# Kernel optimization log

Hardware: AMD Instinct MI355X
Metric: run time of the kernel (lower is better)

The kernel has to match this reference:

```python
import jax, jax.numpy as jnp
import numpy as np

N = 50000        # nodes
E = 800000       # edges (avg degree 16)
NFEAT = 16       # 14 feat + 2 pos
NHID = 64
NCLASS = 1
NGRAPHS = 500
NLAYERS = 5
DT, ALPHA, GAMMA = 1.0, 1.0, 1.0


def _lin_init(k, fan_in, fan_out):
    # torch nn.Linear default: U(-1/sqrt(fan_in), 1/sqrt(fan_in))
    lim = 1.0 / np.sqrt(fan_in)
    kw, kb = jax.random.split(k)
    W = jax.random.uniform(kw, (fan_in, fan_out), minval=-lim, maxval=lim, dtype=jnp.float32)
    b = jax.random.uniform(kb, (fan_out,), minval=-lim, maxval=lim, dtype=jnp.float32)
    return W, b


def setup_inputs() -> dict:
    key = jax.random.key(0)
    ks = jax.random.split(key, 8)
    x = jax.random.normal(ks[0], (N, 14), dtype=jnp.float32)
    pos = jax.random.normal(ks[1], (N, 2), dtype=jnp.float32)
    edge_index = jax.random.randint(ks[2], (2, E), 0, N, dtype=jnp.int64)
    batch = jnp.sort(jax.random.randint(ks[3], (N,), 0, NGRAPHS, dtype=jnp.int64))
    enc_W, enc_b = _lin_init(ks[4], NFEAT, NHID)
    conv_W, conv_b = _lin_init(ks[5], NHID, NHID)
    res_W, res_b = _lin_init(ks[6], NHID, NHID)
    dec_W, dec_b = _lin_init(ks[7], NHID, NCLASS)
    return dict(x=x, pos=pos, edge_index=edge_index, batch=batch,
                enc_W=enc_W, enc_b=enc_b, conv_W=conv_W, conv_b=conv_b,
                res_W=res_W, res_b=res_b, dec_W=dec_W, dec_b=dec_b)


def _gcn_conv(h, src, dst, W, b):
    # PyG GCNConv: add self-loops, symmetric normalization, scatter-add to dst.
    loop = jnp.arange(N, dtype=src.dtype)
    src2 = jnp.concatenate([src, loop])
    dst2 = jnp.concatenate([dst, loop])
    deg = jax.ops.segment_sum(jnp.ones_like(dst2, dtype=h.dtype), dst2, num_segments=N)
    dinv = jnp.where(deg > 0, jax.lax.rsqrt(deg), 0.0)
    hW = h @ W                                   # [N, nhid]
    norm = dinv[src2] * dinv[dst2]               # [E+N]
    msg = hW[src2] * norm[:, None]               # [E+N, nhid]
    return jax.ops.segment_sum(msg, dst2, num_segments=N) + b


def reference(x, pos, edge_index, batch, enc_W, enc_b, conv_W, conv_b, res_W, res_b, dec_W, dec_b):
    src, dst = edge_index[0], edge_index[1]
    inp = jnp.concatenate([x, pos], axis=-1)     # [N, nfeat]
    Y = inp @ enc_W + enc_b
    X = Y
    # dropout p=0 -> identity (eval mode)
    for _ in range(NLAYERS):
        agg = _gcn_conv(X, src, dst, conv_W, conv_b) + (X @ res_W + res_b)
        Y = Y + DT * (jax.nn.relu(agg) - ALPHA * Y - GAMMA * X)
        X = X + DT * Y
    Xo = X @ dec_W + dec_b                       # [N, 1]
    pooled = jax.ops.segment_sum(Xo, batch, num_segments=NGRAPHS)  # [G, 1]
    return pooled.squeeze(-1)                    # [G]
```

## Files before the change

kernel.cpp:

```cpp
#include <hip/hip_runtime.h>

#define NN 50000
#define NE 800000
#define NH 64
#define NG 500
#define NPAD 50176
#define NBKT 782
#define CAP 1536

__device__ __forceinline__ unsigned short f2bf(float f) {
  unsigned x = __float_as_uint(f);
  unsigned r = ((x >> 16) & 1u) + 0x7fffu;
  return (unsigned short)((x + r) >> 16);
}
__device__ __forceinline__ float bf2f(unsigned short u) {
  return __uint_as_float(((unsigned)u) << 16);
}


__global__ __launch_bounds__(256) void k_bin(const int* __restrict__ src, const int* __restrict__ dst,
                                             int* __restrict__ bcur, int* __restrict__ colp) {
  __shared__ int hist[NBKT];
  __shared__ int gbase[NBKT];
  int t = threadIdx.x;
  for (int b = t; b < NBKT; b += 256) hist[b] = 0;
  __syncthreads();
  int e0 = blockIdx.x * 8192;
#pragma unroll
  for (int i = 0; i < 32; i++) {
    int e = e0 + i * 256 + t;
    if (e < NE) atomicAdd(&hist[dst[e] >> 6], 1);
  }
  __syncthreads();
  for (int b = t; b < NBKT; b += 256) {
    int c = hist[b];
    gbase[b] = c ? atomicAdd(&bcur[b], c) : 0;
    hist[b] = 0;
  }
  __syncthreads();
#pragma unroll
  for (int i = 0; i < 32; i++) {
    int e = e0 + i * 256 + t;
    if (e < NE) {
      int s = src[e], d = dst[e];
      int b = d >> 6;
      int r = atomicAdd(&hist[b], 1);
      colp[b * CAP + gbase[b] + r] = (s << 6) | (d & 63);
    }
  }
}


__global__ __launch_bounds__(256) void k_csr(const int* __restrict__ bcur, const int* __restrict__ colp,
                                             int* __restrict__ cols, float* __restrict__ dinv,
                                             int* __restrict__ rowst, int* __restrict__ rowen,
                                             const int* __restrict__ batch, int* __restrict__ gptr) {
  __shared__ int hist[64];
  __shared__ int excl[65];
  int t = threadIdx.x;
  int b = blockIdx.x;

  int tid = b * 256 + t;
  if (tid < NN) {
    int bi = batch[tid];
    int bp = (tid > 0) ? batch[tid - 1] : -1;
    for (int g = bp + 1; g <= bi; g++) gptr[g] = tid;
    if (tid == NN - 1) {
      for (int g = bi + 1; g <= NG; g++) gptr[g] = NN;
    }
  }

  int base = b * CAP;
  int cnt = bcur[b];
  if (t < 64) hist[t] = 0;
  __syncthreads();
  for (int e = t; e < cnt; e += 256) atomicAdd(&hist[colp[base + e] & 63], 1);
  __syncthreads();
  if (t == 0) {
    int run = 0;
#pragma unroll
    for (int i = 0; i < 64; i++) { excl[i] = run; run += hist[i]; }
    excl[64] = run;
  }
  __syncthreads();
  if (t < 64) {
    int n = b * 64 + t;
    rowst[n] = base + excl[t];
    rowen[n] = base + excl[t + 1];
    if (n < NN) dinv[n] = rsqrtf((float)(hist[t] + 1));
    hist[t] = 0;
  }
  __syncthreads();
  for (int e = t; e < cnt; e += 256) {
    int w = colp[base + e];
    int d = w & 63;
    int r = atomicAdd(&hist[d], 1);
    cols[base + excl[d] + r] = w >> 6;
  }
}


__global__ __launch_bounds__(256) void k_encoder(const float* __restrict__ x, const float* __restrict__ pos,
                                                 const float* __restrict__ W, const float* __restrict__ b,
                                                 float* __restrict__ X0) {
  __shared__ float Ws[16 * 64];
  __shared__ float bs[64];
  int t = threadIdx.x;
  for (int i = t; i < 1024; i += 256) Ws[i] = W[i];
  if (t < 64) bs[t] = b[t];
  __syncthreads();
  int n = blockIdx.x * 4 + (t >> 6);
  int h = t & 63;
  if (n >= NN) return;
  float acc = bs[h];
#pragma unroll
  for (int f = 0; f < 14; f++) acc += x[n * 14 + f] * Ws[f * 64 + h];
  acc += pos[n * 2 + 0] * Ws[14 * 64 + h];
  acc += pos[n * 2 + 1] * Ws[15 * 64 + h];
  X0[n * 64 + h] = acc;
}


__global__ __launch_bounds__(256) void k_gemm_dual(const float* __restrict__ Xin,
                                                   const unsigned short* __restrict__ gsum,
                                                   const float* __restrict__ Wc, const float* __restrict__ Wr,
                                                   const float* __restrict__ cb, const float* __restrict__ rb,
                                                   const float* __restrict__ dinv,
                                                   unsigned short* __restrict__ hWbf, float* __restrict__ agg,
                                                   int mode) {
  __shared__ float Xs[64 * 64];
  __shared__ float Wcs[64 * 64];
  __shared__ float Wrs[64 * 64];
  int t = threadIdx.x;
#pragma unroll
  for (int j = 0; j < 4; j++) {
    ((float4*)Wcs)[t + j * 256] = ((const float4*)Wc)[t + j * 256];
    ((float4*)Wrs)[t + j * 256] = ((const float4*)Wr)[t + j * 256];
  }
  int n0 = blockIdx.x * 64;
#pragma unroll
  for (int i = 0; i < 4; i++) {
    int idx = t + i * 256;
    int n = idx >> 4;
    int kg = (idx & 15) << 2;
    float4 v = make_float4(0.f, 0.f, 0.f, 0.f);
    int gn = n0 + n;
    if (gn < NN) {
      v = *(const float4*)(Xin + gn * 64 + kg);
      if (mode) {
        ushort4 g = *(const ushort4*)(gsum + gn * 64 + kg);
        float dvn = dinv[gn];
        v.x = fmaxf(v.x + dvn * bf2f(g.x), 0.f);
        v.y = fmaxf(v.y + dvn * bf2f(g.y), 0.f);
        v.z = fmaxf(v.z + dvn * bf2f(g.z), 0.f);
        v.w = fmaxf(v.w + dvn * bf2f(g.w), 0.f);
      }
    }
    int sw = ((n >> 2) & 7) << 2;
    *(float4*)(Xs + n * 64 + (kg ^ sw)) = v;
  }
  __syncthreads();

  int hg = (t & 15) << 2;
  int ng = t >> 4;
  int nb = ng << 2;
  int swz = (ng & 7) << 2;

  float aC[4][4] = {};
  float aR[4][4] = {};
#pragma unroll 4
  for (int k = 0; k < 64; k++) {
    float4 wc = *(const float4*)(Wcs + k * 64 + hg);
    float4 wr = *(const float4*)(Wrs + k * 64 + hg);
    int kk = k ^ swz;
#pragma unroll
    for (int i = 0; i < 4; i++) {
      float xv = Xs[(nb + i) * 64 + kk];
      aC[i][0] += xv * wc.x; aC[i][1] += xv * wc.y; aC[i][2] += xv * wc.z; aC[i][3] += xv * wc.w;
      aR[i][0] += xv * wr.x; aR[i][1] += xv * wr.y; aR[i][2] += xv * wr.z; aR[i][3] += xv * wr.w;
    }
  }

  float4 cbv = *(const float4*)(cb + hg);
  float4 rbv = *(const float4*)(rb + hg);
#pragma unroll
  for (int i = 0; i < 4; i++) {
    int n = n0 + nb + i;
    if (n < NN) {
      float dv = dinv[n];
      float4 hv;
      hv.x = dv * aC[i][0]; hv.y = dv * aC[i][1]; hv.z = dv * aC[i][2]; hv.w = dv * aC[i][3];
      ushort4 hb;
      hb.x = f2bf(hv.x); hb.y = f2bf(hv.y); hb.z = f2bf(hv.z); hb.w = f2bf(hv.w);
      *(ushort4*)(hWbf + (size_t)n * 64 + hg) = hb;
      float4 av;
      av.x = aR[i][0] + rbv.x + cbv.x + dv * hv.x;
      av.y = aR[i][1] + rbv.y + cbv.y + dv * hv.y;
      av.z = aR[i][2] + rbv.z + cbv.z + dv * hv.z;
      av.w = aR[i][3] + rbv.w + cbv.w + dv * hv.w;
      *(float4*)(agg + n * 64 + hg) = av;
    }
  }
}


__global__ __launch_bounds__(256) void k_gather(const int* __restrict__ rowst, const int* __restrict__ rowen,
                                                const int* __restrict__ cols,
                                                const unsigned short* __restrict__ hWbf,
                                                unsigned short* __restrict__ gsum,
                                                const float* __restrict__ agg, const float* __restrict__ dinv,
                                                const float* __restrict__ decW, float* __restrict__ Xo,
                                                int last) {
  int lane = threadIdx.x & 63;
  int h2 = lane & 31;
  int p = lane >> 5;
  int n = __builtin_amdgcn_readfirstlane(blockIdx.x * 4 + (threadIdx.x >> 6));
  int st = rowst[n];
  int en = rowen[n];
  int deg = en - st;
  float a0 = 0.f, a1 = 0.f;
  for (int base = 0; base < deg; base += 64) {
    int cnt = deg - base;
    if (cnt > 64) cnt = 64;
    int li = lane < cnt ? lane : cnt - 1;
    int colv = cols[st + base + li];
    for (int j = 0; j < cnt; j += 16) {
      int e0 = j + 0 + p, e1 = j + 2 + p, e2 = j + 4 + p, e3 = j + 6 + p;
      int e4 = j + 8 + p, e5 = j + 10 + p, e6 = j + 12 + p, e7 = j + 14 + p;
      int s0 = __shfl(colv, e0 < cnt ? e0 : j, 64);
      int s1 = __shfl(colv, e1 < cnt ? e1 : j, 64);
      int s2 = __shfl(colv, e2 < cnt ? e2 : j, 64);
      int s3 = __shfl(colv, e3 < cnt ? e3 : j, 64);
      int s4 = __shfl(colv, e4 < cnt ? e4 : j, 64);
      int s5 = __shfl(colv, e5 < cnt ? e5 : j, 64);
      int s6 = __shfl(colv, e6 < cnt ? e6 : j, 64);
      int s7 = __shfl(colv, e7 < cnt ? e7 : j, 64);
      unsigned u0 = *(const unsigned*)(hWbf + (size_t)s0 * 64 + h2 * 2);
      unsigned u1 = *(const unsigned*)(hWbf + (size_t)s1 * 64 + h2 * 2);
      unsigned u2 = *(const unsigned*)(hWbf + (size_t)s2 * 64 + h2 * 2);
      unsigned u3 = *(const unsigned*)(hWbf + (size_t)s3 * 64 + h2 * 2);
      unsigned u4 = *(const unsigned*)(hWbf + (size_t)s4 * 64 + h2 * 2);
      unsigned u5 = *(const unsigned*)(hWbf + (size_t)s5 * 64 + h2 * 2);
      unsigned u6 = *(const unsigned*)(hWbf + (size_t)s6 * 64 + h2 * 2);
      unsigned u7 = *(const unsigned*)(hWbf + (size_t)s7 * 64 + h2 * 2);
      a0 += (e0 < cnt) ? bf2f((unsigned short)(u0 & 0xffff)) : 0.f;
      a1 += (e0 < cnt) ? bf2f((unsigned short)(u0 >> 16)) : 0.f;
      a0 += (e1 < cnt) ? bf2f((unsigned short)(u1 & 0xffff)) : 0.f;
      a1 += (e1 < cnt) ? bf2f((unsigned short)(u1 >> 16)) : 0.f;
      a0 += (e2 < cnt) ? bf2f((unsigned short)(u2 & 0xffff)) : 0.f;
      a1 += (e2 < cnt) ? bf2f((unsigned short)(u2 >> 16)) : 0.f;
      a0 += (e3 < cnt) ? bf2f((unsigned short)(u3 & 0xffff)) : 0.f;
      a1 += (e3 < cnt) ? bf2f((unsigned short)(u3 >> 16)) : 0.f;
      a0 += (e4 < cnt) ? bf2f((unsigned short)(u4 & 0xffff)) : 0.f;
      a1 += (e4 < cnt) ? bf2f((unsigned short)(u4 >> 16)) : 0.f;
      a0 += (e5 < cnt) ? bf2f((unsigned short)(u5 & 0xffff)) : 0.f;
      a1 += (e5 < cnt) ? bf2f((unsigned short)(u5 >> 16)) : 0.f;
      a0 += (e6 < cnt) ? bf2f((unsigned short)(u6 & 0xffff)) : 0.f;
      a1 += (e6 < cnt) ? bf2f((unsigned short)(u6 >> 16)) : 0.f;
      a0 += (e7 < cnt) ? bf2f((unsigned short)(u7 & 0xffff)) : 0.f;
      a1 += (e7 < cnt) ? bf2f((unsigned short)(u7 >> 16)) : 0.f;
    }
  }
  a0 += __shfl_down(a0, 32, 64);
  a1 += __shfl_down(a1, 32, 64);
  if (!last) {
    if (lane < 32) {
      unsigned outw = (unsigned)f2bf(a0) | ((unsigned)f2bf(a1) << 16);
      *(unsigned*)(gsum + (size_t)n * 64 + h2 * 2) = outw;
    }
  } else {
    float dv = dinv[n];
    float2 ag = *(const float2*)(agg + (size_t)n * 64 + h2 * 2);
    float xf0 = ag.x + dv * a0;
    float xf1 = ag.y + dv * a1;
    float v = fmaxf(xf0, 0.f) * decW[h2 * 2] + fmaxf(xf1, 0.f) * decW[h2 * 2 + 1];
    v = (lane < 32) ? v : 0.f;
#pragma unroll
    for (int off = 32; off > 0; off >>= 1) v += __shfl_down(v, off, 64);
    if (lane == 0) Xo[n] = v;
  }
}


__global__ __launch_bounds__(256) void k_pool(const float* __restrict__ Xo, const int* __restrict__ gptr,
                                              const float* __restrict__ decb, float* __restrict__ out) {
  __shared__ float part[4];
  int g = blockIdx.x;
  int t = threadIdx.x;
  int st = gptr[g], en = gptr[g + 1];
  float v = 0.f;
  for (int i = st + t; i < en; i += 256) v += Xo[i];
#pragma unroll
  for (int off = 32; off > 0; off >>= 1) v += __shfl_down(v, off, 64);
  if ((t & 63) == 0) part[t >> 6] = v;
  __syncthreads();
  if (t == 0) out[g] = part[0] + part[1] + part[2] + part[3] + (float)(en - st) * decb[0];
}


extern "C" void kernel_launch(void* const* d_in, const int* in_sizes, int n_in,
                              void* d_out, int out_size, void* d_ws, size_t ws_size,
                              hipStream_t stream) {
  (void)in_sizes; (void)n_in; (void)out_size; (void)ws_size;
  const float* x     = (const float*)d_in[0];
  const float* pos   = (const float*)d_in[1];
  const int*   ei    = (const int*)d_in[2];
  const int*   batch = (const int*)d_in[3];
  const float* encW  = (const float*)d_in[4];
  const float* encb  = (const float*)d_in[5];
  const float* convW = (const float*)d_in[6];
  const float* convb = (const float*)d_in[7];
  const float* resW  = (const float*)d_in[8];
  const float* resb  = (const float*)d_in[9];
  const float* decW  = (const float*)d_in[10];
  const float* decb  = (const float*)d_in[11];
  float* out = (float*)d_out;

  const int* src = ei;
  const int* dst = ei + NE;

  float*          ws     = (float*)d_ws;
  float*          dinv   = ws;
  int*            rowst  = (int*)(ws + NPAD);
  int*            rowen  = (int*)(ws + 2 * NPAD);
  int*            bcur   = (int*)(ws + 3 * NPAD);
  int*            gptr   = bcur + 1024;
  float*          Xo     = (float*)(gptr + 512);
  int*            colp   = (int*)(Xo + NPAD);
  int*            cols   = colp + NBKT * CAP;
  unsigned short* hWbf   = (unsigned short*)(cols + NBKT * CAP);
  unsigned short* gsum   = hWbf + (size_t)NPAD * 64;
  float*          bufA   = (float*)(gsum + (size_t)NPAD * 64);
  float*          bufB   = bufA + NN * NH;

  hipMemsetAsync(bcur, 0, 1024 * sizeof(int), stream);

  k_bin<<<(NE + 8191) / 8192, 256, 0, stream>>>(src, dst, bcur, colp);
  k_csr<<<NBKT, 256, 0, stream>>>(bcur, colp, cols, dinv, rowst, rowen, batch, gptr);

  k_encoder<<<(NN + 3) / 4, 256, 0, stream>>>(x, pos, encW, encb, bufA);

  float* aggIn = bufA;
  float* aggOut = bufB;
  for (int l = 0; l < 5; l++) {
    int last = (l == 4) ? 1 : 0;
    k_gemm_dual<<<NBKT, 256, 0, stream>>>(aggIn, gsum, convW, resW, convb, resb, dinv,
                                          hWbf, aggOut, l > 0 ? 1 : 0);
    k_gather<<<NN / 4, 256, 0, stream>>>(rowst, rowen, cols, hWbf, gsum,
                                         aggOut, dinv, decW, Xo, last);
    float* tmp = aggIn; aggIn = aggOut; aggOut = tmp;
  }
  k_pool<<<NG, 256, 0, stream>>>(Xo, gptr, decb, out);
}
```

Before: 327.8 us.

## Use split-bf16 MFMA for dual GEMM with prepacked weight fragments

Replaces the LDS-tiled FP32 FMA dual GEMM with MFMA 16x16x32 bf16 instructions. Activations and weights are each split into high and low bf16 parts, and three cross products are summed to approximate FP32 accuracy. A new prep kernel packs both weight matrices into MFMA fragment layout once, so each wave loads its B fragments straight from global memory and the kernel no longer stages through shared memory. The output stores become scalar 2-byte and 4-byte writes per lane instead of vectorized ones, which may hurt coalescing.

After: 296.8 us. -9.5%, faster.

```diff
diff --git a/kernel.cpp b/kernel.cpp
--- a/kernel.cpp
+++ b/kernel.cpp
@@ -7,6 +7,9 @@
 #define NPAD 50176
 #define NBKT 782
 #define CAP 1536
+
+typedef __attribute__((ext_vector_type(8))) short bf16x8;
+typedef __attribute__((ext_vector_type(4))) float f32x4;
 
 __device__ __forceinline__ unsigned short f2bf(float f) {
   unsigned x = __float_as_uint(f);
@@ -121,84 +124,126 @@
 }
 
 
+__global__ __launch_bounds__(256) void k_wprep(const float* __restrict__ Wc, const float* __restrict__ Wr,
+                                               unsigned short* __restrict__ Wf) {
+  int t = blockIdx.x * 256 + threadIdx.x;
+  if (t >= 2048) return;
+  int fid = t >> 6;
+  int lane = t & 63;
+  int ntile = fid & 3, s = (fid >> 2) & 1, part = (fid >> 3) & 1, mat = fid >> 4;
+  const float* W = mat ? Wr : Wc;
+  int col = ntile * 16 + (lane & 15);
+  int k0 = s * 32 + (lane >> 4) * 8;
+#pragma unroll
+  for (int e = 0; e < 8; e++) {
+    float w = W[(k0 + e) * 64 + col];
+    unsigned short h = f2bf(w);
+    Wf[(size_t)fid * 512 + lane * 8 + e] = part ? f2bf(w - bf2f(h)) : h;
+  }
+}
+
+
 __global__ __launch_bounds__(256) void k_gemm_dual(const float* __restrict__ Xin,
                                                    const unsigned short* __restrict__ gsum,
-                                                   const float* __restrict__ Wc, const float* __restrict__ Wr,
+                                                   const unsigned short* __restrict__ Wf,
                                                    const float* __restrict__ cb, const float* __restrict__ rb,
                                                    const float* __restrict__ dinv,
                                                    unsigned short* __restrict__ hWbf, float* __restrict__ agg,
                                                    int mode) {
-  __shared__ float Xs[64 * 64];
-  __shared__ float Wcs[64 * 64];
-  __shared__ float Wrs[64 * 64];
-  int t = threadIdx.x;
+  int lane = threadIdx.x & 63;
+  int wv = threadIdx.x >> 6;
+  int col16 = lane & 15;
+  int kb = lane >> 4;
+  int n0 = blockIdx.x * 64 + wv * 16;
+
+  int nr = n0 + col16;
+  int nc = nr < NN ? nr : NN - 1;
+  const float* xrow = Xin + (size_t)nc * 64;
+  float v0[8], v1[8];
+  {
+    float4 a = *(const float4*)(xrow + kb * 8);
+    float4 b = *(const float4*)(xrow + kb * 8 + 4);
+    float4 c = *(const float4*)(xrow + 32 + kb * 8);
+    float4 d = *(const float4*)(xrow + 32 + kb * 8 + 4);
+    v0[0] = a.x; v0[1] = a.y; v0[2] = a.z; v0[3] = a.w;
+    v0[4] = b.x; v0[5] = b.y; v0[6] = b.z; v0[7] = b.w;
+    v1[0] = c.x; v1[1] = c.y; v1[2] = c.z; v1[3] = c.w;
+    v1[4] = d.x; v1[5] = d.y; v1[6] = d.z; v1[7] = d.w;
+  }
+  if (mode) {
+    float dvn = dinv[nc];
+    const unsigned* grow = (const unsigned*)(gsum + (size_t)nc * 64);
+    uint4 g0 = *(const uint4*)(grow + kb * 4);
+    uint4 g1 = *(const uint4*)(grow + 16 + kb * 4);
+    unsigned ga[4] = {g0.x, g0.y, g0.z, g0.w};
+    unsigned gb[4] = {g1.x, g1.y, g1.z, g1.w};
+#pragma unroll
+    for (int e = 0; e < 4; e++) {
+      v0[2 * e]     = fmaxf(v0[2 * e]     + dvn * bf2f((unsigned short)(ga[e] & 0xffff)), 0.f);
+      v0[2 * e + 1] = fmaxf(v0[2 * e + 1] + dvn * bf2f((unsigned short)(ga[e] >> 16)), 0.f);
+      v1[2 * e]     = fmaxf(v1[2 * e]     + dvn * bf2f((unsigned short)(gb[e] & 0xffff)), 0.f);
+      v1[2 * e + 1] = fmaxf(v1[2 * e + 1] + dvn * bf2f((unsigned short)(gb[e] >> 16)), 0.f);
+    }
+  }
+  bf16x8 ah0, al0, ah1, al1;
+#pragma unroll
+  for (int e = 0; e < 8; e++) {
+    unsigned short h0 = f2bf(v0[e]);
+    ah0[e] = (short)h0;
+    al0[e] = (short)f2bf(v0[e] - bf2f(h0));
+    unsigned short h1 = f2bf(v1[e]);
+    ah1[e] = (short)h1;
+    al1[e] = (short)f2bf(v1[e] - bf2f(h1));
+  }
+
+  f32x4 aC[4] = {{0.f, 0.f, 0.f, 0.f}, {0.f, 0.f, 0.f, 0.f}, {0.f, 0.f, 0.f, 0.f}, {0.f, 0.f, 0.f, 0.f}};
+  f32x4 aR[4] = {{0.f, 0.f, 0.f, 0.f}, {0.f, 0.f, 0.f, 0.f}, {0.f, 0.f, 0.f, 0.f}, {0.f, 0.f, 0.f, 0.f}};
+  const bf16x8* WFv = (const bf16x8*)Wf;
 #pragma unroll
   for (int j = 0; j < 4; j++) {
-    ((float4*)Wcs)[t + j * 256] = ((const float4*)Wc)[t + j * 256];
-    ((float4*)Wrs)[t + j * 256] = ((const float4*)Wr)[t + j * 256];
-  }
-  int n0 = blockIdx.x * 64;
-#pragma unroll
-  for (int i = 0; i < 4; i++) {
-    int idx = t + i * 256;
-    int n = idx >> 4;
-    int kg = (idx & 15) << 2;
-    float4 v = make_float4(0.f, 0.f, 0.f, 0.f);
-    int gn = n0 + n;
-    if (gn < NN) {
-      v = *(const float4*)(Xin + gn * 64 + kg);
-      if (mode) {
-        ushort4 g = *(const ushort4*)(gsum + gn * 64 + kg);
-        float dvn = dinv[gn];
-        v.x = fmaxf(v.x + dvn * bf2f(g.x), 0.f);
-        v.y = fmaxf(v.y + dvn * bf2f(g.y), 0.f);
-        v.z = fmaxf(v.z + dvn * bf2f(g.z), 0.f);
-        v.w = fmaxf(v.w + dvn * bf2f(g.w), 0.f);
+    bf16x8 wch0 = WFv[(j)      * 64 + lane];
+    bf16x8 wch1 = WFv[(4 + j)  * 64 + lane];
+    bf16x8 wcl0 = WFv[(8 + j)  * 64 + lane];
+    bf16x8 wcl1 = WFv[(12 + j) * 64 + lane];
+    bf16x8 wrh0 = WFv[(16 + j) * 64 + lane];
+    bf16x8 wrh1 = WFv[(20 + j) * 64 + lane];
+    bf16x8 wrl0 = WFv[(24 + j) * 64 + lane];
+    bf16x8 wrl1 = WFv[(28 + j) * 64 + lane];
+    f32x4 c = aC[j];
+    c = __builtin_amdgcn_mfma_f32_16x16x32_bf16(ah0, wch0, c, 0, 0, 0);
+    c = __builtin_amdgcn_mfma_f32_16x16x32_bf16(ah1, wch1, c, 0, 0, 0);
+    c = __builtin_amdgcn_mfma_f32_16x16x32_bf16(al0, wch0, c, 0, 0, 0);
+    c = __builtin_amdgcn_mfma_f32_16x16x32_bf16(al1, wch1, c, 0, 0, 0);
+    c = __builtin_amdgcn_mfma_f32_16x16x32_bf16(ah0, wcl0, c, 0, 0, 0);
+    c = __builtin_amdgcn_mfma_f32_16x16x32_bf16(ah1, wcl1, c, 0, 0, 0);
+    aC[j] = c;
+    f32x4 r = aR[j];
+    r = __builtin_amdgcn_mfma_f32_16x16x32_bf16(ah0, wrh0, r, 0, 0, 0);
+    r = __builtin_amdgcn_mfma_f32_16x16x32_bf16(ah1, wrh1, r, 0, 0, 0);
+    r = __builtin_amdgcn_mfma_f32_16x16x32_bf16(al0, wrh0, r, 0, 0, 0);
+    r = __builtin_amdgcn_mfma_f32_16x16x32_bf16(al1, wrh1, r, 0, 0, 0);
+    r = __builtin_amdgcn_mfma_f32_16x16x32_bf16(ah0, wrl0, r, 0, 0, 0);
+    r = __builtin_amdgcn_mfma_f32_16x16x32_bf16(ah1, wrl1, r, 0, 0, 0);
+    aR[j] = r;
+  }
+
+  float cbv[4], rbv[4];
+#pragma unroll
+  for (int j = 0; j < 4; j++) { cbv[j] = cb[j * 16 + col16]; rbv[j] = rb[j * 16 + col16]; }
+  int rbase = kb * 4;
+#pragma unroll
+  for (int r = 0; r < 4; r++) {
+    int node = n0 + rbase + r;
+    if (node < NN) {
+      float dv = dinv[node];
+      size_t o = (size_t)node * 64 + col16;
+#pragma unroll
+      for (int j = 0; j < 4; j++) {
+        float hc = dv * aC[j][r];
+        unsigned short hb = f2bf(hc);
+        hWbf[o + j * 16] = hb;
+        agg[o + j * 16] = aR[j][r] + rbv[j] + cbv[j] + dv * hc;
       }
-    }
-    int sw = ((n >> 2) & 7) << 2;
-    *(float4*)(Xs + n * 64 + (kg ^ sw)) = v;
-  }
-  __syncthreads();
-
-  int hg = (t & 15) << 2;
-  int ng = t >> 4;
-  int nb = ng << 2;
-  int swz = (ng & 7) << 2;
-
-  float aC[4][4] = {};
-  float aR[4][4] = {};
-#pragma unroll 4
-  for (int k = 0; k < 64; k++) {
-    float4 wc = *(const float4*)(Wcs + k * 64 + hg);
-    float4 wr = *(const float4*)(Wrs + k * 64 + hg);
-    int kk = k ^ swz;
-#pragma unroll
-    for (int i = 0; i < 4; i++) {
-      float xv = Xs[(nb + i) * 64 + kk];
-      aC[i][0] += xv * wc.x; aC[i][1] += xv * wc.y; aC[i][2] += xv * wc.z; aC[i][3] += xv * wc.w;
-      aR[i][0] += xv * wr.x; aR[i][1] += xv * wr.y; aR[i][2] += xv * wr.z; aR[i][3] += xv * wr.w;
-    }
-  }
-
-  float4 cbv = *(const float4*)(cb + hg);
-  float4 rbv = *(const float4*)(rb + hg);
-#pragma unroll
-  for (int i = 0; i < 4; i++) {
-    int n = n0 + nb + i;
-    if (n < NN) {
-      float dv = dinv[n];
-      float4 hv;
-      hv.x = dv * aC[i][0]; hv.y = dv * aC[i][1]; hv.z = dv * aC[i][2]; hv.w = dv * aC[i][3];
-      ushort4 hb;
-      hb.x = f2bf(hv.x); hb.y = f2bf(hv.y); hb.z = f2bf(hv.z); hb.w = f2bf(hv.w);
-      *(ushort4*)(hWbf + (size_t)n * 64 + hg) = hb;
-      float4 av;
-      av.x = aR[i][0] + rbv.x + cbv.x + dv * hv.x;
-      av.y = aR[i][1] + rbv.y + cbv.y + dv * hv.y;
-      av.z = aR[i][2] + rbv.z + cbv.z + dv * hv.z;
-      av.w = aR[i][3] + rbv.w + cbv.w + dv * hv.w;
-      *(float4*)(agg + n * 64 + hg) = av;
     }
   }
 }
@@ -332,9 +377,11 @@
   unsigned short* gsum   = hWbf + (size_t)NPAD * 64;
   float*          bufA   = (float*)(gsum + (size_t)NPAD * 64);
   float*          bufB   = bufA + NN * NH;
+  unsigned short* Wf     = (unsigned short*)(bufB + NN * NH);
 
   hipMemsetAsync(bcur, 0, 1024 * sizeof(int), stream);
 
+  k_wprep<<<8, 256, 0, stream>>>(convW, resW, Wf);
   k_bin<<<(NE + 8191) / 8192, 256, 0, stream>>>(src, dst, bcur, colp);
   k_csr<<<NBKT, 256, 0, stream>>>(bcur, colp, cols, dinv, rowst, rowen, batch, gptr);
 
@@ -344,7 +391,7 @@
   float* aggOut = bufB;
   for (int l = 0; l < 5; l++) {
     int last = (l == 4) ? 1 : 0;
-    k_gemm_dual<<<NBKT, 256, 0, stream>>>(aggIn, gsum, convW, resW, convb, resb, dinv,
+    k_gemm_dual<<<NBKT, 256, 0, stream>>>(aggIn, gsum, Wf, convb, resb, dinv,
                                           hWbf, aggOut, l > 0 ? 1 : 0);
     k_gather<<<NN / 4, 256, 0, stream>>>(rowst, rowen, cols, hWbf, gsum,
                                          aggOut, dinv, decW, Xo, last);
```
